# Optimization experiments

Measured on AMD Instinct MI355X. Metric: run time of the kernel, lower is better.

The kernel has to match this reference:

```python
import jax, jax.numpy as jnp
import numpy as np

DIM = 768

def setup_inputs() -> dict:
    key = jax.random.key(0)
    ks = jax.random.split(key, 11)
    B, N = 4, 2048
    s = 1.0 / np.sqrt(DIM)
    inp = {
        "q": jax.random.normal(ks[0], (B, N, DIM), jnp.float32),
        "k": jax.random.normal(ks[1], (B, N, DIM), jnp.float32),
        "v": jax.random.normal(ks[2], (B, N, DIM), jnp.float32),
        "Wq": jax.random.normal(ks[3], (DIM, DIM), jnp.float32) * s,
        "bq": jnp.zeros((DIM,), jnp.float32),
        "Wk": jax.random.normal(ks[4], (DIM, DIM), jnp.float32) * s,
        "bk": jnp.zeros((DIM,), jnp.float32),
        "Wv": jax.random.normal(ks[5], (DIM, DIM), jnp.float32) * s,
        "bv": jnp.zeros((DIM,), jnp.float32),
        "Wp": jax.random.normal(ks[6], (DIM, DIM), jnp.float32) * s,
        "bp": jnp.zeros((DIM,), jnp.float32),
    }
    return inp

def reference(q, k, v, Wq, bq, Wk, bk, Wv, bv, Wp, bp):
    # Linear projections (torch Linear: x @ W.T + b)
    scale = DIM ** (-0.5)  # note: full dim, num_heads unused in original forward
    qp = q @ Wq.T + bq            # [B, Nq, D]
    kp = k @ Wk.T + bk            # [B, Nk, D]
    vp = v @ Wv.T + bv            # [B, Nk, D]
    attn = jnp.einsum('bqd,bkd->bqk', qp * scale, kp)  # [B, Nq, Nk]
    attn = jax.nn.softmax(attn, axis=-1)
    x = jnp.einsum('bqk,bkd->bqd', attn, vp)           # [B, Nq, D]
    return x @ Wp.T + bp
```

## Files before the change

kernel.cpp:

```cpp
#include <hip/hip_runtime.h>
#include <hip/hip_bf16.h>
#include <math.h>

typedef __bf16 bf16x8 __attribute__((ext_vector_type(8)));
typedef float  f32x4  __attribute__((ext_vector_type(4)));
typedef float  f32x4v __attribute__((ext_vector_type(4)));
typedef unsigned short ushort_t;
typedef ushort_t u16x4 __attribute__((ext_vector_type(4)));
typedef ushort_t u16x8 __attribute__((ext_vector_type(8)));

__device__ __forceinline__ ushort_t f2bf(float f) {
    unsigned u = __builtin_bit_cast(unsigned, f);
    u += 0x7FFFu + ((u >> 16) & 1u);
    return (ushort_t)(u >> 16);
}
__device__ __forceinline__ float bf2f(ushort_t b) {
    return __builtin_bit_cast(float, (unsigned)b << 16);
}

__device__ __forceinline__ void xcd_remap(int& bx, int& by, int& bz) {
    const int gx = gridDim.x, gy = gridDim.y;
    const int nwg = gx * gy * gridDim.z;
    const int lin = (blockIdx.z * gy + blockIdx.y) * gx + blockIdx.x;
    const int chunk = nwg >> 3;
    int nid = (lin & 7) * chunk + (lin >> 3);
    bx = nid % gx; nid /= gx;
    by = nid % gy; bz = nid / gy;
}

__global__ __launch_bounds__(256) void cvt_multi(const float* __restrict__ i0, const float* __restrict__ i1,
                                                 const float* __restrict__ i2, const float* __restrict__ i3,
                                                 ushort_t* __restrict__ o0, ushort_t* __restrict__ o1,
                                                 ushort_t* __restrict__ o2, ushort_t* __restrict__ o3, int n4) {
    const int z = blockIdx.z;
    const float* in  = z == 0 ? i0 : z == 1 ? i1 : z == 2 ? i2 : i3;
    ushort_t*    out = z == 0 ? o0 : z == 1 ? o1 : z == 2 ? o2 : o3;
    int i = blockIdx.x * 256 + threadIdx.x;
    if (i >= n4) return;
    f32x4v v = ((const f32x4v*)in)[i];
    u16x4 o = { f2bf(v.x), f2bf(v.y), f2bf(v.z), f2bf(v.w) };
    ((u16x4*)out)[i] = o;
}

__global__ __launch_bounds__(256) void zero_f32(float* __restrict__ p, int n) {
    int i = blockIdx.x * 256 + threadIdx.x;
    if (i < n) p[i] = 0.f;
}

#define M_SEXP 0
#define M_PVN  1
#define M_OUT  2

#define BM 128
#define BN 128
#define BK 32

#define GEMM_CORE(Ab_, lda_, Bb_, ldb_, Kdim_)                                              \
    __shared__ __align__(16) ushort_t lds[2][2][BM * BK];                                   \
    const int tid  = threadIdx.x;                                                           \
    const int lane = tid & 63;                                                              \
    const int wave = tid >> 6;                                                              \
    const int wr = wave >> 1, wc = wave & 1;                                                \
    f32x4 acc[4][4];                                                                        \
    _Pragma("unroll") for (int i = 0; i < 4; ++i)                                           \
        _Pragma("unroll") for (int j = 0; j < 4; ++j)                                       \
            acc[i][j] = (f32x4){0.f, 0.f, 0.f, 0.f};                                        \
    auto stage = [&](int buf, int kt) {                                                     \
        const int k0 = kt * BK;                                                             \
        _Pragma("unroll") for (int rnd = 0; rnd < 2; ++rnd) {                               \
            const int c    = tid + rnd * 256;                                               \
            const int row  = c >> 2;                                                        \
            const int slot = (c & 3) ^ (row & 3);                                           \
            const ushort_t* ga = (Ab_) + (tM + row) * (long long)(lda_) + k0 + slot * 8;    \
            const ushort_t* gb = (Bb_) + (tN + row) * (long long)(ldb_) + k0 + slot * 8;    \
            ushort_t* la = &lds[buf][0][(rnd * 256 + wave * 64) * 8];                       \
            ushort_t* lb = &lds[buf][1][(rnd * 256 + wave * 64) * 8];                       \
            __builtin_amdgcn_global_load_lds((const __attribute__((address_space(1))) void*)ga, \
                                             (__attribute__((address_space(3))) void*)la, 16, 0, 0); \
            __builtin_amdgcn_global_load_lds((const __attribute__((address_space(1))) void*)gb, \
                                             (__attribute__((address_space(3))) void*)lb, 16, 0, 0); \
        }                                                                                   \
    };                                                                                      \
    auto compute = [&](int buf) {                                                           \
        const int kb  = lane >> 4;                                                          \
        const int r16 = lane & 15;                                                          \
        bf16x8 af[4], bfr[4];                                                               \
        _Pragma("unroll") for (int mi = 0; mi < 4; ++mi) {                                  \
            const int row = wr * 64 + mi * 16 + r16;                                        \
            const int off = row * 64 + ((kb ^ (row & 3)) << 4);                             \
            af[mi] = *(const bf16x8*)((const char*)lds[buf][0] + off);                      \
        }                                                                                   \
        _Pragma("unroll") for (int ni = 0; ni < 4; ++ni) {                                  \
            const int row = wc * 64 + ni * 16 + r16;                                        \
            const int off = row * 64 + ((kb ^ (row & 3)) << 4);                             \
            bfr[ni] = *(const bf16x8*)((const char*)lds[buf][1] + off);                     \
        }                                                                                   \
        _Pragma("unroll") for (int mi = 0; mi < 4; ++mi)                                    \
            _Pragma("unroll") for (int ni = 0; ni < 4; ++ni)                                \
                acc[mi][ni] = __builtin_amdgcn_mfma_f32_16x16x32_bf16(af[mi], bfr[ni], acc[mi][ni], 0, 0, 0); \
    };                                                                                      \
    const int NT = (Kdim_) / BK;                                                            \
    stage(0, 0);                                                                            \
    __syncthreads();                                                                        \
    int cur = 0;                                                                            \
    for (int kt = 0; kt + 1 < NT; ++kt) {                                                   \
        stage(cur ^ 1, kt + 1);                                                             \
        compute(cur);                                                                       \
        __syncthreads();                                                                    \
        cur ^= 1;                                                                           \
    }                                                                                       \
    compute(cur);                                                                           \
    const int rquad = (lane >> 4) * 4;                                                      \
    const int cl    = lane & 15;

template<int MODE>
__global__ __launch_bounds__(256, 3)
void gemm_nt(const ushort_t* __restrict__ A, int lda, long long aBatch,
             const ushort_t* __restrict__ B, int ldb, long long bBatch,
             void* __restrict__ Cv, int ldc, long long cBatch,
             const float* __restrict__ bias, float* __restrict__ rowsum,
             float scale, int K)
{
    int bx, by, bz;
    xcd_remap(bx, by, bz);
    const long long tM = (long long)by * BM;
    const long long tN = (long long)bx * BN;
    const int z = bz;
    const ushort_t* Ab = A + (long long)z * aBatch;
    const ushort_t* Bb = B + (long long)z * bBatch;

    GEMM_CORE(Ab, lda, Bb, ldb, K)

#pragma unroll
    for (int mi = 0; mi < 4; ++mi) {
        const long long r = tM + wr * 64 + mi * 16 + rquad;
        if constexpr (MODE == M_SEXP) {
            ushort_t* out = (ushort_t*)Cv + (long long)z * cBatch;
            float rs[4] = {0.f, 0.f, 0.f, 0.f};
#pragma unroll
            for (int ni = 0; ni < 4; ++ni) {
                f32x4 v = acc[mi][ni];
                const long long c = tN + wc * 64 + ni * 16 + cl;
#pragma unroll
                for (int j = 0; j < 4; ++j) {
                    float p = __expf(v[j] * scale);
                    ushort_t pb = f2bf(p);
                    out[(r + j) * ldc + c] = pb;
                    rs[j] += bf2f(pb);
                }
            }
#pragma unroll
            for (int j = 0; j < 4; ++j) {
                float s = rs[j];
                s += __shfl_xor(s, 1, 64);
                s += __shfl_xor(s, 2, 64);
                s += __shfl_xor(s, 4, 64);
                s += __shfl_xor(s, 8, 64);
                if (cl == 0) atomicAdd(&rowsum[(long long)z * 2048 + r + j], s);
            }
        } else if constexpr (MODE == M_PVN) {
            ushort_t* out = (ushort_t*)Cv + (long long)z * cBatch;
            float inv[4];
#pragma unroll
            for (int j = 0; j < 4; ++j)
                inv[j] = 1.0f / rowsum[(long long)z * 2048 + r + j];
#pragma unroll
            for (int ni = 0; ni < 4; ++ni) {
                f32x4 v = acc[mi][ni];
                const long long c = tN + wc * 64 + ni * 16 + cl;
#pragma unroll
                for (int j = 0; j < 4; ++j)
                    out[(r + j) * ldc + c] = f2bf(v[j] * inv[j]);
            }
        } else {
            float* out = (float*)Cv;
#pragma unroll
            for (int ni = 0; ni < 4; ++ni) {
                f32x4 v = acc[mi][ni];
                const long long c = tN + wc * 64 + ni * 16 + cl;
                const float bc = bias[c];
#pragma unroll
                for (int j = 0; j < 4; ++j)
                    out[(r + j) * ldc + c] = v[j] + bc;
            }
        }
    }
}

__global__ __launch_bounds__(256, 3)
void proj_qkv(const ushort_t* __restrict__ a0, const ushort_t* __restrict__ a1, const ushort_t* __restrict__ a2,
              const ushort_t* __restrict__ w0, const ushort_t* __restrict__ w1, const ushort_t* __restrict__ w2,
              const float* __restrict__ b0, const float* __restrict__ b1, const float* __restrict__ b2,
              ushort_t* __restrict__ dq, ushort_t* __restrict__ dk, ushort_t* __restrict__ dvT)
{
    int bx, by, bz;
    xcd_remap(bx, by, bz);
    const int z = bz;
    const long long tM = (z < 2) ? (long long)by * BM : (long long)bx * BM;
    const long long tN = (z < 2) ? (long long)bx * BN : (long long)by * BN;
    const ushort_t* Ab = z == 0 ? a0 : z == 1 ? a1 : w2;
    const ushort_t* Bb = z == 0 ? w0 : z == 1 ? w1 : a2;
    const float* bias  = z == 0 ? b0 : z == 1 ? b1 : b2;

    GEMM_CORE(Ab, 768, Bb, 768, 768)

#pragma unroll
    for (int mi = 0; mi < 4; ++mi) {
        const long long r = tM + wr * 64 + mi * 16 + rquad;
        if (z < 2) {
            ushort_t* dst = z == 0 ? dq : dk;
#pragma unroll
            for (int ni = 0; ni < 4; ++ni) {
                f32x4 v = acc[mi][ni];
                const long long c = tN + wc * 64 + ni * 16 + cl;
                const float bc = bias[c];
#pragma unroll
                for (int j = 0; j < 4; ++j)
                    dst[(r + j) * 768 + c] = f2bf(v[j] + bc);
            }
        } else {
#pragma unroll
            for (int ni = 0; ni < 4; ++ni) {
                f32x4 v = acc[mi][ni];
                const long long c = tN + wc * 64 + ni * 16 + cl;
#pragma unroll
                for (int j = 0; j < 4; ++j)
                    dvT[(r + j) * 8192 + c] = f2bf(v[j] + bias[r + j]);
            }
        }
    }
}

extern "C" void kernel_launch(void* const* d_in, const int* in_sizes, int n_in,
                              void* d_out, int out_size, void* d_ws, size_t ws_size,
                              hipStream_t stream) {
    (void)in_sizes; (void)n_in; (void)out_size; (void)ws_size;
    const float* q  = (const float*)d_in[0];
    const float* k  = (const float*)d_in[1];
    const float* v  = (const float*)d_in[2];
    const float* Wq = (const float*)d_in[3];
    const float* bq = (const float*)d_in[4];
    const float* Wk = (const float*)d_in[5];
    const float* bk = (const float*)d_in[6];
    const float* Wv = (const float*)d_in[7];
    const float* bv = (const float*)d_in[8];
    const float* Wp = (const float*)d_in[9];
    const float* bp = (const float*)d_in[10];
    float* out = (float*)d_out;

    char* ws = (char*)d_ws;
    ushort_t* qb  = (ushort_t*)(ws);
    ushort_t* kb  = (ushort_t*)(ws + 12582912LL);
    ushort_t* vb  = (ushort_t*)(ws + 25165824LL);
    ushort_t* P   = (ushort_t*)(ws);
    float* rowsum = (float*)(ws + 33554432LL);
    ushort_t* Wqb = (ushort_t*)(ws + 67108864LL);
    ushort_t* Wkb = (ushort_t*)(ws + 68288512LL);
    ushort_t* Wvb = (ushort_t*)(ws + 69468160LL);
    ushort_t* Wpb = (ushort_t*)(ws + 70647808LL);
    ushort_t* qp  = (ushort_t*)(ws + 71827456LL);
    ushort_t* kp  = (ushort_t*)(ws + 84410368LL);
    ushort_t* vpT = (ushort_t*)(ws + 96993280LL);
    ushort_t* Ob  = qp;

    const float scale = 1.0f / sqrtf(768.0f);

    cvt_multi<<<dim3(6144, 1, 3), 256, 0, stream>>>(q, k, v, nullptr, qb, kb, vb, nullptr, 1572864);
    cvt_multi<<<dim3(576, 1, 4), 256, 0, stream>>>(Wq, Wk, Wv, Wp, Wqb, Wkb, Wvb, Wpb, 147456);

    proj_qkv<<<dim3(6, 64, 3), 256, 0, stream>>>(qb, kb, vb, Wqb, Wkb, Wvb, bq, bk, bv, qp, kp, vpT);

    zero_f32<<<32, 256, 0, stream>>>(rowsum, 8192);

    gemm_nt<M_SEXP><<<dim3(16, 16, 4), 256, 0, stream>>>(qp, 768, 1572864, kp, 768, 1572864,
                                                         P, 2048, 4194304, nullptr, rowsum, scale, 768);

    gemm_nt<M_PVN><<<dim3(6, 16, 4), 256, 0, stream>>>(P, 2048, 4194304, vpT, 8192, 2048,
                                                       Ob, 768, 1572864, nullptr, rowsum, 1.0f, 2048);

    gemm_nt<M_OUT><<<dim3(6, 64, 1), 256, 0, stream>>>(Ob, 768, 0, Wpb, 768, 0, out, 768, 0, bp, nullptr, 1.0f, 768);
}
```

Before: 166.1 us.

## Use 256x256 tiled GEMM with direct-to-LDS loads for projection and QK^T

Adds a new GEMM core with 256x256 output tiles, 8 waves, BK=64, XOR-swizzled LDS, global_load_lds async copies and MFMA priority hints. The QKV projection and the QK^T exp kernel now use it in place of the 128x128 core. The goal is more data reuse per tile and less load-instruction overhead. The cost is much smaller grids: the projection drops to 288 blocks and QK^T to 256 blocks, which may underfill the CUs, and each thread holds a larger accumulator, adding register pressure.

```diff
diff --git a/kernel.cpp b/kernel.cpp
--- a/kernel.cpp
+++ b/kernel.cpp
@@ -47,7 +47,153 @@
     if (i < n) p[i] = 0.f;
 }
 
-#define M_SEXP 0
+#define GEMM256_CORE(Ab_, lda_, Bb_, ldb_, Kdim_)                                           \
+    __shared__ __align__(16) ushort_t lds[2][2][2][128 * 64];                               \
+    const int tid  = threadIdx.x;                                                           \
+    const int lane = tid & 63;                                                              \
+    const int wave = tid >> 6;                                                              \
+    const int wm = wave >> 2, wn = wave & 3;                                                \
+    const int r16 = lane & 15, kb = lane >> 4;                                              \
+    f32x4 acc[8][4];                                                                        \
+    _Pragma("unroll") for (int i = 0; i < 8; ++i)                                           \
+        _Pragma("unroll") for (int j = 0; j < 4; ++j)                                       \
+            acc[i][j] = (f32x4){0.f, 0.f, 0.f, 0.f};                                        \
+    auto stage = [&](int kt) {                                                              \
+        const int d  = kt & 1;                                                              \
+        const int k0 = kt * 64;                                                             \
+        _Pragma("unroll") for (int arr = 0; arr < 2; ++arr)                                 \
+        _Pragma("unroll") for (int h = 0; h < 2; ++h)                                       \
+        _Pragma("unroll") for (int l = 0; l < 2; ++l) {                                     \
+            const int idx = l * 512 + tid;                                                  \
+            const int row = idx >> 3, sl = idx & 7;                                         \
+            const int ssrc = sl ^ (row & 7);                                                \
+            const long long grow = h * 128 + row;                                           \
+            const ushort_t* g = (arr == 0)                                                  \
+                ? (Ab_) + (tM + grow) * (long long)(lda_) + k0 + ssrc * 8                   \
+                : (Bb_) + (tN + grow) * (long long)(ldb_) + k0 + ssrc * 8;                  \
+            ushort_t* lp = &lds[d][arr][h][idx * 8];                                        \
+            __builtin_amdgcn_global_load_lds((const __attribute__((address_space(1))) void*)g, \
+                                             (__attribute__((address_space(3))) void*)lp, 16, 0, 0); \
+        }                                                                                   \
+    };                                                                                      \
+    auto compute = [&](int kt) {                                                            \
+        const int d = kt & 1;                                                               \
+        _Pragma("unroll") for (int kk = 0; kk < 2; ++kk) {                                  \
+            bf16x8 bfr[4];                                                                  \
+            _Pragma("unroll") for (int ni = 0; ni < 4; ++ni) {                              \
+                const int row = (wn & 1) * 64 + ni * 16 + r16;                              \
+                const int o16 = row * 8 + ((kk * 4 + kb) ^ (row & 7));                      \
+                bfr[ni] = *(const bf16x8*)((const char*)&lds[d][1][wn >> 1][0] + o16 * 16); \
+            }                                                                               \
+            __builtin_amdgcn_s_setprio(1);                                                  \
+            _Pragma("unroll") for (int mi = 0; mi < 8; ++mi) {                              \
+                const int row = mi * 16 + r16;                                              \
+                const int o16 = row * 8 + ((kk * 4 + kb) ^ (row & 7));                      \
+                bf16x8 af = *(const bf16x8*)((const char*)&lds[d][0][wm][0] + o16 * 16);    \
+                _Pragma("unroll") for (int ni = 0; ni < 4; ++ni)                            \
+                    acc[mi][ni] = __builtin_amdgcn_mfma_f32_16x16x32_bf16(af, bfr[ni], acc[mi][ni], 0, 0, 0); \
+            }                                                                               \
+            __builtin_amdgcn_s_setprio(0);                                                  \
+        }                                                                                   \
+    };                                                                                      \
+    const int NT = (Kdim_) / 64;                                                            \
+    stage(0);                                                                               \
+    __syncthreads();                                                                        \
+    for (int t = 0; t < NT; ++t) {                                                          \
+        if (t + 1 < NT) stage(t + 1);                                                       \
+        compute(t);                                                                         \
+        __syncthreads();                                                                    \
+    }                                                                                       \
+    const int rquad = (lane >> 4) * 4;                                                      \
+    const int cl    = lane & 15;
+
+__global__ __launch_bounds__(512, 2)
+void sexp256(const ushort_t* __restrict__ qp, const ushort_t* __restrict__ kp,
+             ushort_t* __restrict__ P, float* __restrict__ rowsum, float scale)
+{
+    int bx, by, bz;
+    xcd_remap(bx, by, bz);
+    const long long tM = (long long)by * 256;
+    const long long tN = (long long)bx * 256;
+    const int z = bz;
+    const ushort_t* Ab = qp + (long long)z * 1572864;
+    const ushort_t* Bb = kp + (long long)z * 1572864;
+
+    GEMM256_CORE(Ab, 768, Bb, 768, 768)
+
+    ushort_t* out = P + (long long)z * 4194304;
+#pragma unroll
+    for (int mi = 0; mi < 8; ++mi) {
+        const long long r = tM + wm * 128 + mi * 16 + rquad;
+        float rs[4] = {0.f, 0.f, 0.f, 0.f};
+#pragma unroll
+        for (int ni = 0; ni < 4; ++ni) {
+            f32x4 v = acc[mi][ni];
+            const long long c = tN + wn * 64 + ni * 16 + cl;
+#pragma unroll
+            for (int j = 0; j < 4; ++j) {
+                float p = __expf(v[j] * scale);
+                ushort_t pb = f2bf(p);
+                out[(r + j) * 2048 + c] = pb;
+                rs[j] += bf2f(pb);
+            }
+        }
+#pragma unroll
+        for (int j = 0; j < 4; ++j) {
+            float s = rs[j];
+            s += __shfl_xor(s, 1, 64);
+            s += __shfl_xor(s, 2, 64);
+            s += __shfl_xor(s, 4, 64);
+            s += __shfl_xor(s, 8, 64);
+            if (cl == 0) atomicAdd(&rowsum[(long long)z * 2048 + r + j], s);
+        }
+    }
+}
+
+__global__ __launch_bounds__(512, 2)
+void proj256(const ushort_t* __restrict__ a0, const ushort_t* __restrict__ a1, const ushort_t* __restrict__ a2,
+             const ushort_t* __restrict__ w0, const ushort_t* __restrict__ w1, const ushort_t* __restrict__ w2,
+             const float* __restrict__ b0, const float* __restrict__ b1, const float* __restrict__ b2,
+             ushort_t* __restrict__ dq, ushort_t* __restrict__ dk, ushort_t* __restrict__ dvT)
+{
+    int bx, by, bz;
+    xcd_remap(bx, by, bz);
+    const int z = bz;
+    const long long tM = (z < 2) ? (long long)by * 256 : (long long)bx * 256;
+    const long long tN = (z < 2) ? (long long)bx * 256 : (long long)by * 256;
+    const ushort_t* Ab = z == 0 ? a0 : z == 1 ? a1 : w2;
+    const ushort_t* Bb = z == 0 ? w0 : z == 1 ? w1 : a2;
+    const float* bias  = z == 0 ? b0 : z == 1 ? b1 : b2;
+
+    GEMM256_CORE(Ab, 768, Bb, 768, 768)
+
+#pragma unroll
+    for (int mi = 0; mi < 8; ++mi) {
+        const long long r = tM + wm * 128 + mi * 16 + rquad;
+        if (z < 2) {
+            ushort_t* dst = z == 0 ? dq : dk;
+#pragma unroll
+            for (int ni = 0; ni < 4; ++ni) {
+                f32x4 v = acc[mi][ni];
+                const long long c = tN + wn * 64 + ni * 16 + cl;
+                const float bc = bias[c];
+#pragma unroll
+                for (int j = 0; j < 4; ++j)
+                    dst[(r + j) * 768 + c] = f2bf(v[j] + bc);
+            }
+        } else {
+#pragma unroll
+            for (int ni = 0; ni < 4; ++ni) {
+                f32x4 v = acc[mi][ni];
+                const long long c = tN + wn * 64 + ni * 16 + cl;
+#pragma unroll
+                for (int j = 0; j < 4; ++j)
+                    dvT[(r + j) * 8192 + c] = f2bf(v[j] + bias[r + j]);
+            }
+        }
+    }
+}
+
 #define M_PVN  1
 #define M_OUT  2
 
@@ -119,7 +265,7 @@
              const ushort_t* __restrict__ B, int ldb, long long bBatch,
              void* __restrict__ Cv, int ldc, long long cBatch,
              const float* __restrict__ bias, float* __restrict__ rowsum,
-             float scale, int K)
+             int K)
 {
     int bx, by, bz;
     xcd_remap(bx, by, bz);
@@ -134,31 +280,7 @@
 #pragma unroll
     for (int mi = 0; mi < 4; ++mi) {
         const long long r = tM + wr * 64 + mi * 16 + rquad;
-        if constexpr (MODE == M_SEXP) {
-            ushort_t* out = (ushort_t*)Cv + (long long)z * cBatch;
-            float rs[4] = {0.f, 0.f, 0.f, 0.f};
-#pragma unroll
-            for (int ni = 0; ni < 4; ++ni) {
-                f32x4 v = acc[mi][ni];
-                const long long c = tN + wc * 64 + ni * 16 + cl;
-#pragma unroll
-                for (int j = 0; j < 4; ++j) {
-                    float p = __expf(v[j] * scale);
-                    ushort_t pb = f2bf(p);
-                    out[(r + j) * ldc + c] = pb;
-                    rs[j] += bf2f(pb);
-                }
-            }
-#pragma unroll
-            for (int j = 0; j < 4; ++j) {
-                float s = rs[j];
-                s += __shfl_xor(s, 1, 64);
-                s += __shfl_xor(s, 2, 64);
-                s += __shfl_xor(s, 4, 64);
-                s += __shfl_xor(s, 8, 64);
-                if (cl == 0) atomicAdd(&rowsum[(long long)z * 2048 + r + j], s);
-            }
-        } else if constexpr (MODE == M_PVN) {
+        if constexpr (MODE == M_PVN) {
             ushort_t* out = (ushort_t*)Cv + (long long)z * cBatch;
             float inv[4];
 #pragma unroll
@@ -182,50 +304,6 @@
 #pragma unroll
                 for (int j = 0; j < 4; ++j)
                     out[(r + j) * ldc + c] = v[j] + bc;
-            }
-        }
-    }
-}
-
-__global__ __launch_bounds__(256, 3)
-void proj_qkv(const ushort_t* __restrict__ a0, const ushort_t* __restrict__ a1, const ushort_t* __restrict__ a2,
-              const ushort_t* __restrict__ w0, const ushort_t* __restrict__ w1, const ushort_t* __restrict__ w2,
-              const float* __restrict__ b0, const float* __restrict__ b1, const float* __restrict__ b2,
-              ushort_t* __restrict__ dq, ushort_t* __restrict__ dk, ushort_t* __restrict__ dvT)
-{
-    int bx, by, bz;
-    xcd_remap(bx, by, bz);
-    const int z = bz;
-    const long long tM = (z < 2) ? (long long)by * BM : (long long)bx * BM;
-    const long long tN = (z < 2) ? (long long)bx * BN : (long long)by * BN;
-    const ushort_t* Ab = z == 0 ? a0 : z == 1 ? a1 : w2;
-    const ushort_t* Bb = z == 0 ? w0 : z == 1 ? w1 : a2;
-    const float* bias  = z == 0 ? b0 : z == 1 ? b1 : b2;
-
-    GEMM_CORE(Ab, 768, Bb, 768, 768)
-
-#pragma unroll
-    for (int mi = 0; mi < 4; ++mi) {
-        const long long r = tM + wr * 64 + mi * 16 + rquad;
-        if (z < 2) {
-            ushort_t* dst = z == 0 ? dq : dk;
-#pragma unroll
-            for (int ni = 0; ni < 4; ++ni) {
-                f32x4 v = acc[mi][ni];
-                const long long c = tN + wc * 64 + ni * 16 + cl;
-                const float bc = bias[c];
-#pragma unroll
-                for (int j = 0; j < 4; ++j)
-                    dst[(r + j) * 768 + c] = f2bf(v[j] + bc);
-            }
-        } else {
-#pragma unroll
-            for (int ni = 0; ni < 4; ++ni) {
-                f32x4 v = acc[mi][ni];
-                const long long c = tN + wc * 64 + ni * 16 + cl;
-#pragma unroll
-                for (int j = 0; j < 4; ++j)
-                    dvT[(r + j) * 8192 + c] = f2bf(v[j] + bias[r + j]);
             }
         }
     }
@@ -268,15 +346,14 @@
     cvt_multi<<<dim3(6144, 1, 3), 256, 0, stream>>>(q, k, v, nullptr, qb, kb, vb, nullptr, 1572864);
     cvt_multi<<<dim3(576, 1, 4), 256, 0, stream>>>(Wq, Wk, Wv, Wp, Wqb, Wkb, Wvb, Wpb, 147456);
 
-    proj_qkv<<<dim3(6, 64, 3), 256, 0, stream>>>(qb, kb, vb, Wqb, Wkb, Wvb, bq, bk, bv, qp, kp, vpT);
+    proj256<<<dim3(3, 32, 3), 512, 0, stream>>>(qb, kb, vb, Wqb, Wkb, Wvb, bq, bk, bv, qp, kp, vpT);
 
     zero_f32<<<32, 256, 0, stream>>>(rowsum, 8192);
 
-    gemm_nt<M_SEXP><<<dim3(16, 16, 4), 256, 0, stream>>>(qp, 768, 1572864, kp, 768, 1572864,
-                                                         P, 2048, 4194304, nullptr, rowsum, scale, 768);
+    sexp256<<<dim3(8, 8, 4), 512, 0, stream>>>(qp, kp, P, rowsum, scale);
 
     gemm_nt<M_PVN><<<dim3(6, 16, 4), 256, 0, stream>>>(P, 2048, 4194304, vpT, 8192, 2048,
-                                                       Ob, 768, 1572864, nullptr, rowsum, 1.0f, 2048);
-
-    gemm_nt<M_OUT><<<dim3(6, 64, 1), 256, 0, stream>>>(Ob, 768, 0, Wpb, 768, 0, out, 768, 0, bp, nullptr, 1.0f, 768);
-}
+                                                       Ob, 768, 1572864, nullptr, rowsum, 2048);
+
+    gemm_nt<M_OUT><<<dim3(6, 64, 1), 256, 0, stream>>>(Ob, 768, 0, Wpb, 768, 0, out, 768, 0, bp, nullptr, 768);
+}
```

Result: no change. 169.2 us (+1.9%).
